# Kernel tuning notes

Hardware: AMD Instinct MI355X
Metric: run time of the kernel (lower is better)

Reference implementation:

```python
import jax, jax.numpy as jnp
import numpy as np

_EPS = 1e-5
_I48 = float(1.0 / np.sqrt(48.0))
_I16 = float(1.0 / np.sqrt(16.0))
# fully-connected TP paths (mul_in, mul_out) for hidden(48x0e+48x1o+16x1e) x sh(0e+1e+2e) -> hidden
_PATHS = [(48, 48), (48, 16), (48, 48), (48, 48), (48, 48), (16, 16), (16, 48), (16, 16), (16, 16)]
_NW = sum(i * o for i, o in _PATHS)  # 11520


def _ln(x, g, b):
    mu = x.mean(-1, keepdims=True)
    var = ((x - mu) ** 2).mean(-1, keepdims=True)
    return g * (x - mu) * jax.lax.rsqrt(var + _EPS) + b


def _split(W):
    out, off = [], 0
    for i, o in _PATHS:
        out.append(W[:, off:off + i * o].reshape(-1, i, o))
        off += i * o
    return out


def _forward(protein_coords, protein_features, ligand_coords, ligand_features, t,
             te_w1, te_b1, te_w2, te_b2, te_ln_g, te_ln_b,
             pe_w1, pe_b1, pe_ln_g, pe_ln_b, pe_w2, pe_b2,
             le_w1, le_b1, le_ln_g, le_ln_b, le_w2, le_b2,
             sp_w, sp_b, emb_w, ee_w1, ee_b1, ee_w2, ee_b2,
             conv_w1, conv_b1, conv_w2, conv_b2, conv_w3, conv_b3,
             bn_gs, bn_bs, bn_gv, bn_gw, si_ws, si_wv, si_ww,
             out_ws, out_wv, edge_src, edge_dst):
    Nl = ligand_coords.shape[0]
    Np = protein_coords.shape[0]
    N = Nl + Np
    E = edge_src.shape[0]
    silu = jax.nn.silu

    # sinusoidal time embedding -> Linear/SiLU/Linear/LayerNorm
    half = 32
    freq = jnp.exp(jnp.arange(half, dtype=jnp.float32) * (-np.log(10000.0) / (half - 1)))
    emb = t[:, None] * freq[None, :]
    emb = jnp.concatenate([jnp.sin(emb), jnp.cos(emb)], -1)  # (1, 64)
    temb = _ln(silu(emb @ te_w1 + te_b1) @ te_w2 + te_b2, te_ln_g, te_ln_b)

    # scalar node encoders (dropout = eval identity)
    protein_ca = protein_coords[:, 0, :]
    ph = silu(_ln(protein_features @ pe_w1 + pe_b1, pe_ln_g, pe_ln_b)) @ pe_w2 + pe_b2
    lh = silu(_ln(ligand_features @ le_w1 + le_b1, le_ln_g, le_ln_b)) @ le_w2 + le_b2

    # edge geometry (ligand -> protein) + spherical harmonics in Cartesian form
    vec = ligand_coords[edge_src] - protein_ca[edge_dst]  # (E, 3)
    dist = jnp.sqrt((vec ** 2).sum(-1) + 1e-12)
    n = vec / dist[:, None]  # unit vector = l=1 SH
    Q = n[:, :, None] * n[:, None, :] - jnp.eye(3, dtype=n.dtype) / 3.0  # l=2 SH (traceless sym)
    te_exp = jnp.broadcast_to(temb[0], (E, temb.shape[-1]))
    ef = silu(jnp.concatenate([dist[:, None], te_exp], -1) @ ee_w1 + ee_b1) @ ee_w2 + ee_b2  # (E, 32)

    # input embedding: scalars only feed 0e; 1o/1e channels start at zero
    comb = jnp.concatenate([lh, ph], 0) @ sp_w + sp_b  # (N, 48)
    s = (comb @ emb_w) * _I48
    v = jnp.zeros((N, 48, 3), s.dtype)
    w = jnp.zeros((N, 16, 3), s.dtype)

    dst_n = edge_dst + Nl
    deg = jax.ops.segment_sum(jnp.ones((E,), s.dtype), dst_n, N).clip(1.0)

    for i in range(conv_w1.shape[0]):
        # edge MLP -> per-edge fully-connected tensor-product weights
        m = silu(ef @ conv_w1[i] + conv_b1[i])
        m = silu(m @ conv_w2[i] + conv_b2[i])
        Wt = m @ conv_w3[i] + conv_b3[i]  # (E, 11520)
        Wss, Wsw, Wv0, Wv1, Wv2, Ww0, Wws, Ww1, Ww2 = _split(Wt)

        se, ve, we = s[edge_src], v[edge_src], w[edge_src]
        wn = jnp.einsum('eid,ed->ei', we, n)        # 1e x 1e -> 0e (dot)
        cv = jnp.cross(ve, n[:, None, :])           # 1o x 1e -> 1o (cross)
        cw = jnp.cross(we, n[:, None, :])           # 1e x 1e -> 1e (cross)
        qv = jnp.einsum('edc,eic->eid', Q, ve)      # 1o x 2e -> 1o
        qw = jnp.einsum('edc,eic->eid', Q, we)      # 1e x 2e -> 1e

        m_s = jnp.einsum('eio,ei->eo', Wss, se) * _I48 + jnp.einsum('eio,ei->eo', Wws, wn) * _I16
        m_v = (jnp.einsum('eio,eid->eod', Wv0, ve) + jnp.einsum('eio,eid->eod', Wv1, cv)
               + jnp.einsum('eio,eid->eod', Wv2, qv)) * _I48
        m_w = jnp.einsum('eio,ei,ed->eod', Wsw, se, n) * _I48 + (
            jnp.einsum('eio,eid->eod', Ww0, we) + jnp.einsum('eio,eid->eod', Ww1, cw)
            + jnp.einsum('eio,eid->eod', Ww2, qw)) * _I16

        # scatter-mean to destination nodes
        S = jax.ops.segment_sum(m_s, dst_n, N) / deg[:, None]
        V = jax.ops.segment_sum(m_v, dst_n, N) / deg[:, None, None]
        Wm = jax.ops.segment_sum(m_w, dst_n, N) / deg[:, None, None]

        # self interaction (per-irrep linear)
        a_s = S + (s @ si_ws[i]) * _I48
        a_v = V + jnp.einsum('io,nid->nod', si_wv[i], v) * _I48
        a_w = Wm + jnp.einsum('io,nid->nod', si_ww[i], w) * _I16

        # equivariant batch norm (batch statistics)
        mu = a_s.mean(0)
        var = ((a_s - mu) ** 2).mean(0)
        n_s = bn_gs[i] * (a_s - mu) * jax.lax.rsqrt(var + _EPS) + bn_bs[i]
        n_v = a_v * (bn_gv[i] * jax.lax.rsqrt((a_v ** 2).sum(-1).mean(0) + _EPS))[None, :, None]
        n_w = a_w * (bn_gw[i] * jax.lax.rsqrt((a_w ** 2).sum(-1).mean(0) + _EPS))[None, :, None]

        s, v, w = s + n_s, v + n_v, w + n_w

    feats = (s[:Nl] @ out_ws) * _I48                          # (Nl, 256)
    out_v = jnp.einsum('io,nid->nod', out_wv, v[:Nl]) * _I48  # (Nl, 3, 3)
    vf = out_v.mean(1)                                        # vector_field (Nl, 3)
    return jnp.concatenate([vf, feats], -1)                   # (Nl, 259)


def setup_inputs():
    key = jax.random.key(0)
    ks = iter(jax.random.split(key, 80))
    f32 = jnp.float32

    def nrm(shape, scale=1.0):
        return jax.random.normal(next(ks), shape, f32) * scale

    def lin(fi, fo, lead=()):
        return nrm(lead + (fi, fo), 1.0 / np.sqrt(fi)), jnp.zeros(lead + (fo,), f32)

    Nl, Np, E, L = 2048, 4096, 8192, 6
    inp = {}
    inp['protein_coords'] = nrm((Np, 2, 3), 5.0)
    inp['protein_features'] = nrm((Np, 96))
    inp['ligand_coords'] = nrm((Nl, 3), 5.0)
    inp['ligand_features'] = nrm((Nl, 52))
    inp['t'] = jax.random.uniform(next(ks), (1,), f32)
    inp['te_w1'], inp['te_b1'] = lin(64, 128)
    inp['te_w2'], inp['te_b2'] = lin(128, 64)
    inp['te_ln_g'], inp['te_ln_b'] = jnp.ones((64,), f32), jnp.zeros((64,), f32)
    inp['pe_w1'], inp['pe_b1'] = lin(96, 128)
    inp['pe_ln_g'], inp['pe_ln_b'] = jnp.ones((128,), f32), jnp.zeros((128,), f32)
    inp['pe_w2'], inp['pe_b2'] = lin(128, 48)
    inp['le_w1'], inp['le_b1'] = lin(52, 128)
    inp['le_ln_g'], inp['le_ln_b'] = jnp.ones((128,), f32), jnp.zeros((128,), f32)
    inp['le_w2'], inp['le_b2'] = lin(128, 48)
    inp['sp_w'], inp['sp_b'] = lin(48, 48)
    inp['emb_w'] = nrm((48, 48))
    inp['ee_w1'], inp['ee_b1'] = lin(65, 32)
    inp['ee_w2'], inp['ee_b2'] = lin(32, 32)
    inp['conv_w1'], inp['conv_b1'] = lin(32, 128, (L,))
    inp['conv_w2'], inp['conv_b2'] = lin(128, 128, (L,))
    inp['conv_w3'], inp['conv_b3'] = lin(128, _NW, (L,))
    inp['bn_gs'], inp['bn_bs'] = jnp.ones((L, 48), f32), jnp.zeros((L, 48), f32)
    inp['bn_gv'], inp['bn_gw'] = jnp.ones((L, 48), f32), jnp.ones((L, 16), f32)
    inp['si_ws'] = nrm((L, 48, 48))
    inp['si_wv'] = nrm((L, 48, 48))
    inp['si_ww'] = nrm((L, 16, 16))
    inp['out_ws'] = nrm((48, 256))
    inp['out_wv'] = nrm((48, 3))
    inp['edge_src'] = jax.random.randint(next(ks), (E,), 0, Nl)
    inp['edge_dst'] = jax.random.randint(next(ks), (E,), 0, Np)
    return inp


def reference(protein_coords, protein_features, ligand_coords, ligand_features, t,
              te_w1, te_b1, te_w2, te_b2, te_ln_g, te_ln_b,
              pe_w1, pe_b1, pe_ln_g, pe_ln_b, pe_w2, pe_b2,
              le_w1, le_b1, le_ln_g, le_ln_b, le_w2, le_b2,
              sp_w, sp_b, emb_w, ee_w1, ee_b1, ee_w2, ee_b2,
              conv_w1, conv_b1, conv_w2, conv_b2, conv_w3, conv_b3,
              bn_gs, bn_bs, bn_gv, bn_gw, si_ws, si_wv, si_ww,
              out_ws, out_wv, edge_src, edge_dst):
    return _forward(protein_coords, protein_features, ligand_coords, ligand_features, t,
                    te_w1, te_b1, te_w2, te_b2, te_ln_g, te_ln_b,
                    pe_w1, pe_b1, pe_ln_g, pe_ln_b, pe_w2, pe_b2,
                    le_w1, le_b1, le_ln_g, le_ln_b, le_w2, le_b2,
                    sp_w, sp_b, emb_w, ee_w1, ee_b1, ee_w2, ee_b2,
                    conv_w1, conv_b1, conv_w2, conv_b2, conv_w3, conv_b3,
                    bn_gs, bn_bs, bn_gv, bn_gw, si_ws, si_wv, si_ww,
                    out_ws, out_wv, edge_src, edge_dst)
```

## Files before the change

kernel.cpp:

```cpp
#include <hip/hip_runtime.h>
#include <hip/hip_bf16.h>
#include <math.h>

#define I48 0.14433756729740643f
#define NKB 194
#define KCH 4
#define KSPL 6

typedef __attribute__((ext_vector_type(8))) _Float16 half8;
typedef __attribute__((ext_vector_type(4))) float f32x4;

__device__ __forceinline__ float silu_f(float x){ return x / (1.f + __expf(-x)); }

__global__ void k_temb(const float* __restrict__ t_in,
                       const float* __restrict__ w1, const float* __restrict__ b1,
                       const float* __restrict__ w2, const float* __restrict__ b2,
                       const float* __restrict__ g,  const float* __restrict__ b,
                       float* __restrict__ temb){
  __shared__ float emb[64], h1[128], red[128];
  __shared__ float s_mu, s_rs;
  int t = threadIdx.x;
  float tv = t_in[0];
  if (t < 64){
    int i = t & 31;
    float fr = __expf((float)i * (-9.210340371976184f/31.f));
    float a = tv * fr;
    emb[t] = (t < 32) ? sinf(a) : cosf(a);
  }
  __syncthreads();
  {
    float z = b1[t];
    for (int i=0;i<64;i++) z += emb[i]*w1[i*128+t];
    h1[t] = silu_f(z);
  }
  __syncthreads();
  float tp = 0.f;
  if (t < 64){
    tp = b2[t];
    for (int j=0;j<128;j++) tp += h1[j]*w2[j*64+t];
  }
  red[t] = (t<64)? tp : 0.f;
  __syncthreads();
  for (int st=64;st;st>>=1){ if(t<st) red[t]+=red[t+st]; __syncthreads(); }
  if (t==0) s_mu = red[0]/64.f;
  __syncthreads();
  float d = tp - s_mu;
  red[t] = (t<64)? d*d : 0.f;
  __syncthreads();
  for (int st=64;st;st>>=1){ if(t<st) red[t]+=red[t+st]; __syncthreads(); }
  if (t==0) s_rs = rsqrtf(red[0]/64.f + 1e-5f);
  __syncthreads();
  if (t<64) temb[t] = g[t]*(d*s_rs) + b[t];
}

__global__ void k_encs0(const float* __restrict__ x, int in_dim,
                        const float* __restrict__ w1, const float* __restrict__ b1,
                        const float* __restrict__ g,  const float* __restrict__ bb,
                        const float* __restrict__ w2, const float* __restrict__ b2,
                        const float* __restrict__ spw, const float* __restrict__ spb,
                        const float* __restrict__ embw,
                        float* __restrict__ s, int row_off){
  __shared__ float sx[96], sh[128], red[128], vout[48], c48[48];
  __shared__ float s_mu, s_rs;
  int row = blockIdx.x, t = threadIdx.x;
  for (int i=t;i<in_dim;i+=128) sx[i] = x[(size_t)row*in_dim+i];
  __syncthreads();
  float z = b1[t];
  for (int i=0;i<in_dim;i++) z += sx[i]*w1[i*128+t];
  red[t]=z; __syncthreads();
  for (int st=64;st;st>>=1){ if(t<st) red[t]+=red[t+st]; __syncthreads(); }
  if(!t) s_mu = red[0]/128.f;
  __syncthreads();
  float d = z - s_mu;
  red[t]=d*d; __syncthreads();
  for (int st=64;st;st>>=1){ if(t<st) red[t]+=red[t+st]; __syncthreads(); }
  if(!t) s_rs = rsqrtf(red[0]/128.f+1e-5f);
  __syncthreads();
  float h = g[t]*(d*s_rs)+bb[t];
  sh[t] = silu_f(h);
  __syncthreads();
  if (t<48){
    float o = b2[t];
    for (int j=0;j<128;j++) o += sh[j]*w2[j*48+t];
    vout[t] = o;
  }
  __syncthreads();
  if (t<48){
    float c = spb[t];
    for (int i=0;i<48;i++) c += vout[i]*spw[i*48+t];
    c48[t] = c;
  }
  __syncthreads();
  if (t<48){
    float v = 0.f;
    for (int i=0;i<48;i++) v += c48[i]*embw[i*48+t];
    s[(size_t)(row_off+row)*48+t] = v*I48;
  }
}

__global__ void k_edge(const float* __restrict__ lc, const float* __restrict__ pc,
                       const int* __restrict__ src, const int* __restrict__ dst,
                       const float* __restrict__ temb,
                       const float* __restrict__ w1, const float* __restrict__ b1,
                       const float* __restrict__ w2, const float* __restrict__ b2,
                       float* __restrict__ ef, float* __restrict__ degf,
                       int E, int Nl){
  __shared__ float sh_h[2][32];
  int t = threadIdx.x, sub = t>>5, j = t&31;
  int e = blockIdx.x*2 + sub;
  if (e < E){
    int s_ = src[e], d_ = dst[e];
    float vx = lc[(size_t)s_*3+0]-pc[(size_t)d_*6+0];
    float vy = lc[(size_t)s_*3+1]-pc[(size_t)d_*6+1];
    float vz = lc[(size_t)s_*3+2]-pc[(size_t)d_*6+2];
    float dist = sqrtf(vx*vx+vy*vy+vz*vz+1e-12f);
    float h = b1[j] + dist*w1[j];
    for (int a=0;a<64;a++) h += temb[a]*w1[(a+1)*32+j];
    sh_h[sub][j] = silu_f(h);
  }
  __syncthreads();
  if (e < E){
    float o = b2[j];
    for (int a=0;a<32;a++) o += sh_h[sub][a]*w2[a*32+j];
    ef[(size_t)e*32+j] = o;
    if (j==0) atomicAdd(&degf[Nl + dst[e]], 1.f);
  }
}

__global__ void k_packMLP(const float* __restrict__ w1, const float* __restrict__ w2,
                          _Float16* __restrict__ w1p, _Float16* __restrict__ w2p, int L){
  int tot1 = L*8*512;
  int tot2 = L*32*512;
  int total = tot1 + tot2;
  for (int idx = blockIdx.x*blockDim.x+threadIdx.x; idx < total; idx += gridDim.x*blockDim.x){
    if (idx < tot1){
      int j = idx & 7, lane = (idx>>3)&63, rest = idx>>9;
      int nt = rest & 7, l = rest >> 3;
      int k = (lane>>4)*8 + j, o = nt*16 + (lane&15);
      w1p[idx] = (_Float16)w1[((size_t)l*32 + k)*128 + o];
    } else {
      int i2 = idx - tot1;
      int j = i2 & 7, lane = (i2>>3)&63, rest = i2>>9;
      int nt = rest & 7, kb = (rest>>3)&3, l = rest >> 5;
      int k = kb*32 + (lane>>4)*8 + j, o = nt*16 + (lane&15);
      w2p[i2] = (_Float16)w2[((size_t)l*128 + k)*128 + o];
    }
  }
}

__global__ __launch_bounds__(256) void k_mlp2(
    const float* __restrict__ ef,
    const _Float16* __restrict__ w1p, const float* __restrict__ b1a,
    const _Float16* __restrict__ w2p, const float* __restrict__ b2a,
    _Float16* __restrict__ m2h, int E){
  __shared__ __align__(16) _Float16 sef[64][40];
  __shared__ __align__(16) _Float16 shh[64][136];
  __shared__ float sb1[128], sb2[128];
  const int t = threadIdx.x, lane = t & 63, w = t >> 6;
  const int e0 = blockIdx.x * 64;
  const int l  = blockIdx.y;
  const _Float16* w1l = w1p + (size_t)l*4096;
  const _Float16* w2l = w2p + (size_t)l*16384;
  if (t < 128) sb1[t] = b1a[l*128 + t];
  else         sb2[t-128] = b2a[l*128 + (t-128)];
  {
    int row = t >> 2, g = t & 3;
    const float* p = ef + ((size_t)(e0+row))*32 + g*8;
    float4 p0 = *(const float4*)p, p1 = *(const float4*)(p+4);
    half8 hv;
    hv[0]=(_Float16)p0.x; hv[1]=(_Float16)p0.y; hv[2]=(_Float16)p0.z; hv[3]=(_Float16)p0.w;
    hv[4]=(_Float16)p1.x; hv[5]=(_Float16)p1.y; hv[6]=(_Float16)p1.z; hv[7]=(_Float16)p1.w;
    *(half8*)&sef[row][g*8] = hv;
  }
  __syncthreads();
  const int m = lane & 15, quad = lane >> 4;
  const int r = w*16 + m;
  half8 a1 = *(const half8*)&sef[r][quad*8];
  f32x4 acc1[8];
  #pragma unroll
  for (int nt=0; nt<8; nt++){
    half8 b = *(const half8*)(w1l + (nt*64 + lane)*8);
    f32x4 z = {0.f,0.f,0.f,0.f};
    acc1[nt] = __builtin_amdgcn_mfma_f32_16x16x32_f16(a1, b, z, 0,0,0);
  }
  #pragma unroll
  for (int nt=0; nt<8; nt++){
    float bv = sb1[nt*16 + m];
    #pragma unroll
    for (int rr=0; rr<4; rr++)
      shh[w*16 + quad*4 + rr][nt*16 + m] = (_Float16)silu_f(acc1[nt][rr] + bv);
  }
  __syncthreads();
  f32x4 acc2[8];
  #pragma unroll
  for (int nt=0;nt<8;nt++) acc2[nt] = (f32x4){0.f,0.f,0.f,0.f};
  #pragma unroll
  for (int kb=0; kb<4; kb++){
    half8 a2 = *(const half8*)&shh[r][kb*32 + quad*8];
    #pragma unroll
    for (int nt=0; nt<8; nt++){
      half8 b = *(const half8*)(w2l + ((size_t)(kb*8+nt)*64 + lane)*8);
      acc2[nt] = __builtin_amdgcn_mfma_f32_16x16x32_f16(a2, b, acc2[nt], 0,0,0);
    }
  }
  __syncthreads();
  #pragma unroll
  for (int nt=0; nt<8; nt++){
    float bv = sb2[nt*16 + m];
    #pragma unroll
    for (int rr=0; rr<4; rr++)
      shh[w*16 + quad*4 + rr][nt*16 + m] = (_Float16)silu_f(acc2[nt][rr] + bv);
  }
  __syncthreads();
  for (int q = t; q < 64*16; q += 256){
    int row = q >> 4, c = q & 15;
    half8 hv = *(const half8*)&shh[row][c*8];
    *(half8*)(m2h + ((size_t)l*E + e0 + row)*128 + c*8) = hv;
  }
}

__global__ void k_packB2(const float* __restrict__ w3, const float* __restrict__ b3,
                         _Float16* __restrict__ wbh, int L){
  int tot1 = L*128*2304;
  int tot2 = L*64*48;
  int total = tot1 + tot2;
  for (int idx = blockIdx.x*blockDim.x+threadIdx.x; idx < total; idx += gridDim.x*blockDim.x){
    if (idx < tot1){
      int r = idx % 2304; int q = idx / 2304;
      int kk = q & 127;   int l = q >> 7;
      float v = w3[(size_t)(l*128+kk)*11520 + r];
      int i = r / 48, o = r - i*48;
      int kp = i*128 + kk;
      int kblk = kp >> 5, p = kp & 31;
      int lane = ((p>>3)<<4) + (o & 15);
      int j = p & 7;
      int nt = o >> 4;
      wbh[((((size_t)l*NKB + kblk)*3 + nt)*64 + lane)*8 + j] = (_Float16)v;
    } else {
      int i2 = idx - tot1;
      int o = i2 % 48; int q = i2 / 48;
      int ii = q & 63; int l = q >> 6;
      float v = (ii < 48) ? b3[(size_t)l*11520 + ii*48 + o] : 0.f;
      int kp = 6144 + ii;
      int kblk = kp >> 5, p = kp & 31;
      int lane = ((p>>3)<<4) + (o & 15);
      int j = p & 7;
      int nt = o >> 4;
      wbh[((((size_t)l*NKB + kblk)*3 + nt)*64 + lane)*8 + j] = (_Float16)v;
    }
  }
}

__global__ __launch_bounds__(256) void k_msg6(
    const _Float16* __restrict__ m2h, const float* __restrict__ s,
    const float* __restrict__ a_s, const float* __restrict__ bnlp,
    const float* __restrict__ gp, const float* __restrict__ bp, int apply, int N,
    const _Float16* __restrict__ wbh,
    const int* __restrict__ src, const int* __restrict__ dst,
    float* __restrict__ Sacc, int Nl){
  __shared__ __align__(16) _Float16 sB[2][KCH*1536];
  __shared__ __align__(16) _Float16 sseq[128][72];
  __shared__ int sdst[128];
  __shared__ float ksc[48], kbs[48];
  const int t = threadIdx.x, lane = t & 63, w = t >> 6;
  const int e0 = blockIdx.x * 128;
  const int by = blockIdx.y;
  const int kb0 = by*32;
  const int kb1 = (by==KSPL-1) ? NKB : kb0+32;

  if (t < 48){
    if (apply){
      float su = bnlp[t], sq = bnlp[48+t];
      float mu  = su/(float)N;
      float var = sq/(float)N - mu*mu;
      float r = rsqrtf(var + 1e-5f);
      float sc = gp[t]*r;
      ksc[t] = sc; kbs[t] = bp[t] - mu*sc;
    } else { ksc[t]=0.f; kbs[t]=0.f; }
  }
  if (t < 128) sdst[t] = dst[e0+t];
  __syncthreads();

  for (int q = t; q < 128*9; q += 256){
    int e = q/9, g = q - e*9;
    half8 hv = {};
    if (g < 6){
      size_t base = (size_t)src[e0+e]*48 + g*8;
      const float* sp = s + base;
      if (apply){
        const float* ap = a_s + base;
        #pragma unroll
        for (int j=0;j<8;j++){
          int o = g*8+j;
          hv[j] = (_Float16)(sp[j] + ap[j]*ksc[o] + kbs[o]);
        }
      } else {
        #pragma unroll
        for (int j=0;j<8;j++) hv[j] = (_Float16)sp[j];
      }
    }
    *(half8*)&sseq[e][g*8] = hv;
  }

  const int m = lane & 15, quad = lane >> 4;
  const int r0 = w*32 + m, r1 = r0 + 16;

  half8 f0[4], f1[4];
  {
    const _Float16* base0 = m2h + (size_t)(e0+r0)*128 + quad*8;
    const _Float16* base1 = m2h + (size_t)(e0+r1)*128 + quad*8;
    #pragma unroll
    for (int sub=0; sub<4; sub++){
      f0[sub] = *(const half8*)(base0 + sub*32);
      f1[sub] = *(const half8*)(base1 + sub*32);
    }
  }

  auto stage = [&](int c){
    int kbase = kb0 + c*KCH;
    int nk = kb1 - kbase; if (nk > KCH) nk = KCH;
    int bytes = nk*3072;
    const char* g = (const char*)wbh + (size_t)kbase*3072;
    char* lb = (char*)sB[c&1];
    for (int off = w*1024; off < bytes; off += 4096){
      __builtin_amdgcn_global_load_lds(
        (const __attribute__((address_space(1))) void*)(g + off + (size_t)lane*16),
        (__attribute__((address_space(3))) void*)(lb + off), 16, 0, 0);
    }
  };
  stage(0);

  f32x4 acc00={0.f,0.f,0.f,0.f}, acc01={0.f,0.f,0.f,0.f}, acc02={0.f,0.f,0.f,0.f};
  f32x4 acc10={0.f,0.f,0.f,0.f}, acc11={0.f,0.f,0.f,0.f}, acc12={0.f,0.f,0.f,0.f};

  const int nch = (kb1-kb0+KCH-1)/KCH;
  for (int c = 0; c < nch; c++){
    __syncthreads();
    if (c+1 < nch) stage(c+1);
    int kbase = kb0 + c*KCH;
    int kbn = kb1 - kbase; if (kbn > KCH) kbn = KCH;
    const _Float16* bb = sB[c&1];
    if (kbn == KCH && kbase < 192){
      int i = kbase >> 2;
      _Float16 sv0 = sseq[r0][i], sv1 = sseq[r1][i];
      half8 s0v = {sv0,sv0,sv0,sv0,sv0,sv0,sv0,sv0};
      half8 s1v = {sv1,sv1,sv1,sv1,sv1,sv1,sv1,sv1};
      #pragma unroll
      for (int kk = 0; kk < KCH; kk++){
        half8 a0 = f0[kk] * s0v;
        half8 a1 = f1[kk] * s1v;
        const _Float16* bk = bb + kk*1536 + lane*8;
        half8 b0 = *(const half8*)(bk);
        half8 b1 = *(const half8*)(bk + 512);
        half8 b2 = *(const half8*)(bk + 1024);
        acc00 = __builtin_amdgcn_mfma_f32_16x16x32_f16(a0, b0, acc00, 0, 0, 0);
        acc01 = __builtin_amdgcn_mfma_f32_16x16x32_f16(a0, b1, acc01, 0, 0, 0);
        acc02 = __builtin_amdgcn_mfma_f32_16x16x32_f16(a0, b2, acc02, 0, 0, 0);
        acc10 = __builtin_amdgcn_mfma_f32_16x16x32_f16(a1, b0, acc10, 0, 0, 0);
        acc11 = __builtin_amdgcn_mfma_f32_16x16x32_f16(a1, b1, acc11, 0, 0, 0);
        acc12 = __builtin_amdgcn_mfma_f32_16x16x32_f16(a1, b2, acc12, 0, 0, 0);
      }
    } else {
      for (int kk = 0; kk < kbn; kk++){
        int kblk = kbase + kk;
        int ib = ((kblk-192) << 5) + quad*8;
        half8 a0 = *(const half8*)&sseq[r0][ib];
        half8 a1 = *(const half8*)&sseq[r1][ib];
        const _Float16* bk = bb + kk*1536 + lane*8;
        half8 b0 = *(const half8*)(bk);
        half8 b1 = *(const half8*)(bk + 512);
        half8 b2 = *(const half8*)(bk + 1024);
        acc00 = __builtin_amdgcn_mfma_f32_16x16x32_f16(a0, b0, acc00, 0, 0, 0);
        acc01 = __builtin_amdgcn_mfma_f32_16x16x32_f16(a0, b1, acc01, 0, 0, 0);
        acc02 = __builtin_amdgcn_mfma_f32_16x16x32_f16(a0, b2, acc02, 0, 0, 0);
        acc10 = __builtin_amdgcn_mfma_f32_16x16x32_f16(a1, b0, acc10, 0, 0, 0);
        acc11 = __builtin_amdgcn_mfma_f32_16x16x32_f16(a1, b1, acc11, 0, 0, 0);
        acc12 = __builtin_amdgcn_mfma_f32_16x16x32_f16(a1, b2, acc12, 0, 0, 0);
      }
    }
  }
  #pragma unroll
  for (int r = 0; r < 4; r++){
    int el0 = w*32 + quad*4 + r;
    int el1 = el0 + 16;
    float* p0 = Sacc + (size_t)(Nl + sdst[el0])*48 + m;
    float* p1 = Sacc + (size_t)(Nl + sdst[el1])*48 + m;
    atomicAdd(p0 +  0, acc00[r]*I48);
    atomicAdd(p0 + 16, acc01[r]*I48);
    atomicAdd(p0 + 32, acc02[r]*I48);
    atomicAdd(p1 +  0, acc10[r]*I48);
    atomicAdd(p1 + 16, acc11[r]*I48);
    atomicAdd(p1 + 32, acc12[r]*I48);
  }
}

__global__ __launch_bounds__(256) void k_node3(float* __restrict__ Sacc,
                       const float* __restrict__ degf,
                       float* __restrict__ s, const float* __restrict__ siw,
                       float* __restrict__ a_s,
                       const float* __restrict__ bnlp, const float* __restrict__ gp,
                       const float* __restrict__ bp, int apply,
                       float* __restrict__ bnl, int N){
  __shared__ float sh_s[16][48];
  __shared__ float sw[2304];
  __shared__ float csum[48], csq[48];
  __shared__ float ksc[48], kbs[48];
  int t = threadIdx.x;
  int n0 = blockIdx.x*16;
  if (t < 48){
    if (apply){
      float su = bnlp[t], sq = bnlp[48+t];
      float mu  = su/(float)N;
      float var = sq/(float)N - mu*mu;
      float r = rsqrtf(var + 1e-5f);
      float sc = gp[t]*r;
      ksc[t] = sc; kbs[t] = bp[t] - mu*sc;
    } else { ksc[t]=0.f; kbs[t]=0.f; }
    csum[t]=0.f; csq[t]=0.f;
  }
  for (int q=t;q<2304;q+=256) sw[q] = siw[q];
  __syncthreads();
  for (int q=t;q<768;q+=256){
    int nl=q/48, o=q-nl*48;
    size_t idx = (size_t)(n0+nl)*48+o;
    float v = s[idx];
    if (apply){
      v += a_s[idx]*ksc[o] + kbs[o];
      s[idx] = v;
    }
    sh_s[nl][o] = v;
  }
  __syncthreads();
  int nl = t>>4;
  int ob = (t&15)*3;
  int n = n0+nl;
  float dg = degf[n]; if (dg < 1.f) dg = 1.f;
  float inv = 1.f/dg;
  #pragma unroll
  for (int j=0;j<3;j++){
    int o = ob+j;
    size_t idx = (size_t)n*48+o;
    float acc = 0.f;
    for (int i=0;i<48;i++) acc += sh_s[nl][i]*sw[i*48+o];
    float a = Sacc[idx]*inv + acc*I48;
    Sacc[idx] = 0.f;
    a_s[idx] = a;
    atomicAdd(&csum[o], a);
    atomicAdd(&csq[o], a*a);
  }
  __syncthreads();
  if (t<96) atomicAdd(&bnl[t], (t<48) ? csum[t] : csq[t-48]);
}

__global__ void k_out2(const float* __restrict__ s, const float* __restrict__ a_s,
                       const float* __restrict__ bnlp, const float* __restrict__ gp,
                       const float* __restrict__ bp, int N,
                       const float* __restrict__ ows, float* __restrict__ out){
  __shared__ float sh_s[48];
  __shared__ float ksc[48], kbs[48];
  int n = blockIdx.x, t = threadIdx.x;
  if (t < 48){
    float su = bnlp[t], sq = bnlp[48+t];
    float mu  = su/(float)N;
    float var = sq/(float)N - mu*mu;
    float r = rsqrtf(var + 1e-5f);
    float sc = gp[t]*r;
    ksc[t] = sc; kbs[t] = bp[t] - mu*sc;
  }
  __syncthreads();
  if (t<48){
    size_t idx = (size_t)n*48+t;
    sh_s[t] = s[idx] + a_s[idx]*ksc[t] + kbs[t];
  }
  __syncthreads();
  float acc = 0.f;
  for (int i=0;i<48;i++) acc += sh_s[i]*ows[i*256+t];
  out[(size_t)n*259 + 3 + t] = acc*I48;
  if (t<3) out[(size_t)n*259 + t] = 0.f;
}

extern "C" void kernel_launch(void* const* d_in, const int* in_sizes, int n_in,
                              void* d_out, int out_size, void* d_ws, size_t ws_size,
                              hipStream_t stream){
  const float* protein_coords   = (const float*)d_in[0];
  const float* protein_features = (const float*)d_in[1];
  const float* ligand_coords    = (const float*)d_in[2];
  const float* ligand_features  = (const float*)d_in[3];
  const float* t_in    = (const float*)d_in[4];
  const float* te_w1   = (const float*)d_in[5];
  const float* te_b1   = (const float*)d_in[6];
  const float* te_w2   = (const float*)d_in[7];
  const float* te_b2   = (const float*)d_in[8];
  const float* te_ln_g = (const float*)d_in[9];
  const float* te_ln_b = (const float*)d_in[10];
  const float* pe_w1   = (const float*)d_in[11];
  const float* pe_b1   = (const float*)d_in[12];
  const float* pe_ln_g = (const float*)d_in[13];
  const float* pe_ln_b = (const float*)d_in[14];
  const float* pe_w2   = (const float*)d_in[15];
  const float* pe_b2   = (const float*)d_in[16];
  const float* le_w1   = (const float*)d_in[17];
  const float* le_b1   = (const float*)d_in[18];
  const float* le_ln_g = (const float*)d_in[19];
  const float* le_ln_b = (const float*)d_in[20];
  const float* le_w2   = (const float*)d_in[21];
  const float* le_b2   = (const float*)d_in[22];
  const float* sp_w    = (const float*)d_in[23];
  const float* sp_b    = (const float*)d_in[24];
  const float* emb_w   = (const float*)d_in[25];
  const float* ee_w1   = (const float*)d_in[26];
  const float* ee_b1   = (const float*)d_in[27];
  const float* ee_w2   = (const float*)d_in[28];
  const float* ee_b2   = (const float*)d_in[29];
  const float* conv_w1 = (const float*)d_in[30];
  const float* conv_b1 = (const float*)d_in[31];
  const float* conv_w2 = (const float*)d_in[32];
  const float* conv_b2 = (const float*)d_in[33];
  const float* conv_w3 = (const float*)d_in[34];
  const float* conv_b3 = (const float*)d_in[35];
  const float* bn_gs   = (const float*)d_in[36];
  const float* bn_bs   = (const float*)d_in[37];
  const float* si_ws   = (const float*)d_in[40];
  const float* out_ws  = (const float*)d_in[43];
  const int* edge_src  = (const int*)d_in[45];
  const int* edge_dst  = (const int*)d_in[46];

  int Np = in_sizes[0]/6;
  int Nl = in_sizes[2]/3;
  int E  = in_sizes[45];
  int N  = Nl+Np;
  int L  = in_sizes[36]/48;

  float* W = (float*)d_ws;
  size_t off = 0;
  auto alloc = [&](size_t n)->float*{ float* p = W+off; off += (n+63)&~(size_t)63; return p; };
  float* degf  = alloc(N);
  float* Sacc  = alloc((size_t)N*48);
  float* bnb   = alloc((size_t)L*96);
  float* temb  = alloc(64);
  float* sbuf  = alloc((size_t)N*48);
  float* ef    = alloc((size_t)E*32);
  float* a_s   = alloc((size_t)N*48);
  _Float16* m2h = (_Float16*)alloc((size_t)L*E*128/2 + 64);
  _Float16* wbh = (_Float16*)alloc((size_t)L*NKB*1536/2 + 64);
  _Float16* w1p = (_Float16*)alloc((size_t)L*4096/2 + 64);
  _Float16* w2p = (_Float16*)alloc((size_t)L*16384/2 + 64);

  hipMemsetAsync(degf, 0, ((size_t)N + (size_t)N*48 + (size_t)L*96 + 192)*sizeof(float), stream);
  k_packB2<<<2048,256,0,stream>>>(conv_w3, conv_b3, wbh, L);
  k_packMLP<<<480,256,0,stream>>>(conv_w1, conv_w2, w1p, w2p, L);
  k_temb<<<1,128,0,stream>>>(t_in, te_w1, te_b1, te_w2, te_b2, te_ln_g, te_ln_b, temb);
  k_encs0<<<Np,128,0,stream>>>(protein_features, 96, pe_w1, pe_b1, pe_ln_g, pe_ln_b,
                               pe_w2, pe_b2, sp_w, sp_b, emb_w, sbuf, Nl);
  k_encs0<<<Nl,128,0,stream>>>(ligand_features, 52, le_w1, le_b1, le_ln_g, le_ln_b,
                               le_w2, le_b2, sp_w, sp_b, emb_w, sbuf, 0);
  k_edge<<<(E+1)/2,64,0,stream>>>(ligand_coords, protein_coords, edge_src, edge_dst, temb,
                                  ee_w1, ee_b1, ee_w2, ee_b2, ef, degf, E, Nl);
  dim3 mlpg(E/64, L);
  k_mlp2<<<mlpg,256,0,stream>>>(ef, w1p, conv_b1, w2p, conv_b2, m2h, E);

  dim3 mgrid(E/128, KSPL);
  for (int l=0;l<L;l++){
    const float* bnlp = (l>0) ? (bnb + (l-1)*96) : bnb;
    const float* gp   = (l>0) ? (bn_gs + (l-1)*48) : bn_gs;
    const float* bp   = (l>0) ? (bn_bs + (l-1)*48) : bn_bs;
    int apply = (l>0) ? 1 : 0;
    k_msg6<<<mgrid,256,0,stream>>>(m2h + (size_t)l*E*128, sbuf, a_s, bnlp, gp, bp, apply, N,
                                   wbh + (size_t)l*NKB*1536, edge_src, edge_dst, Sacc, Nl);
    k_node3<<<N/16,256,0,stream>>>(Sacc, degf, sbuf, si_ws + (size_t)l*2304, a_s,
                                   bnlp, gp, bp, apply, bnb + l*96, N);
  }
  k_out2<<<Nl,256,0,stream>>>(sbuf, a_s, bnb + (L-1)*96, bn_gs + (L-1)*48, bn_bs + (L-1)*48,
                              N, out_ws, (float*)d_out);
}
```

Before: 463.1 us.

## Halve message-kernel edge tile and merge pack and encoder launches

The message kernel now processes 64 edges per block instead of 128, with one 16-row MFMA tile per wave, which doubles the grid and lowers register and LDS use per block. Two weight-packing kernels are merged into one launch, and the protein and ligand encoders become a single launch that selects weights per row. This trades more parallel blocks and fewer launches for twice the staging of the B weights per edge, since each weight chunk is now reused across fewer edges.

```diff
diff --git a/kernel.cpp b/kernel.cpp
--- a/kernel.cpp
+++ b/kernel.cpp
@@ -53,17 +53,28 @@
   if (t<64) temb[t] = g[t]*(d*s_rs) + b[t];
 }
 
-__global__ void k_encs0(const float* __restrict__ x, int in_dim,
-                        const float* __restrict__ w1, const float* __restrict__ b1,
-                        const float* __restrict__ g,  const float* __restrict__ bb,
-                        const float* __restrict__ w2, const float* __restrict__ b2,
-                        const float* __restrict__ spw, const float* __restrict__ spb,
-                        const float* __restrict__ embw,
-                        float* __restrict__ s, int row_off){
+__global__ void k_encall(const float* __restrict__ pf, const float* __restrict__ lf, int Nl,
+    const float* __restrict__ pw1, const float* __restrict__ pb1,
+    const float* __restrict__ pg,  const float* __restrict__ pbb,
+    const float* __restrict__ pw2, const float* __restrict__ pb2,
+    const float* __restrict__ lw1, const float* __restrict__ lb1,
+    const float* __restrict__ lg,  const float* __restrict__ lbb,
+    const float* __restrict__ lw2, const float* __restrict__ lb2,
+    const float* __restrict__ spw, const float* __restrict__ spb,
+    const float* __restrict__ embw, float* __restrict__ s){
   __shared__ float sx[96], sh[128], red[128], vout[48], c48[48];
   __shared__ float s_mu, s_rs;
   int row = blockIdx.x, t = threadIdx.x;
-  for (int i=t;i<in_dim;i+=128) sx[i] = x[(size_t)row*in_dim+i];
+  bool lig = row < Nl;
+  int in_dim = lig ? 52 : 96;
+  const float* x  = lig ? (lf + (size_t)row*52) : (pf + (size_t)(row-Nl)*96);
+  const float* w1 = lig ? lw1 : pw1;
+  const float* b1 = lig ? lb1 : pb1;
+  const float* g  = lig ? lg  : pg;
+  const float* bb = lig ? lbb : pbb;
+  const float* w2 = lig ? lw2 : pw2;
+  const float* b2 = lig ? lb2 : pb2;
+  for (int i=t;i<in_dim;i+=128) sx[i] = x[i];
   __syncthreads();
   float z = b1[t];
   for (int i=0;i<in_dim;i++) z += sx[i]*w1[i*128+t];
@@ -94,7 +105,7 @@
   if (t<48){
     float v = 0.f;
     for (int i=0;i<48;i++) v += c48[i]*embw[i*48+t];
-    s[(size_t)(row_off+row)*48+t] = v*I48;
+    s[(size_t)row*48+t] = v*I48;
   }
 }
 
@@ -127,23 +138,50 @@
   }
 }
 
-__global__ void k_packMLP(const float* __restrict__ w1, const float* __restrict__ w2,
+__global__ void k_packAll(const float* __restrict__ w3, const float* __restrict__ b3,
+                          const float* __restrict__ w1, const float* __restrict__ w2,
+                          _Float16* __restrict__ wbh,
                           _Float16* __restrict__ w1p, _Float16* __restrict__ w2p, int L){
-  int tot1 = L*8*512;
-  int tot2 = L*32*512;
-  int total = tot1 + tot2;
+  int tot1 = L*128*2304;
+  int tot2 = L*64*48;
+  int tot3 = L*8*512;
+  int tot4 = L*32*512;
+  int total = tot1 + tot2 + tot3 + tot4;
   for (int idx = blockIdx.x*blockDim.x+threadIdx.x; idx < total; idx += gridDim.x*blockDim.x){
     if (idx < tot1){
-      int j = idx & 7, lane = (idx>>3)&63, rest = idx>>9;
+      int r = idx % 2304; int q = idx / 2304;
+      int kk = q & 127;   int l = q >> 7;
+      float v = w3[(size_t)(l*128+kk)*11520 + r];
+      int i = r / 48, o = r - i*48;
+      int kp = i*128 + kk;
+      int kblk = kp >> 5, p = kp & 31;
+      int lane = ((p>>3)<<4) + (o & 15);
+      int j = p & 7;
+      int nt = o >> 4;
+      wbh[((((size_t)l*NKB + kblk)*3 + nt)*64 + lane)*8 + j] = (_Float16)v;
+    } else if (idx < tot1 + tot2){
+      int i2 = idx - tot1;
+      int o = i2 % 48; int q = i2 / 48;
+      int ii = q & 63; int l = q >> 6;
+      float v = (ii < 48) ? b3[(size_t)l*11520 + ii*48 + o] : 0.f;
+      int kp = 6144 + ii;
+      int kblk = kp >> 5, p = kp & 31;
+      int lane = ((p>>3)<<4) + (o & 15);
+      int j = p & 7;
+      int nt = o >> 4;
+      wbh[((((size_t)l*NKB + kblk)*3 + nt)*64 + lane)*8 + j] = (_Float16)v;
+    } else if (idx < tot1 + tot2 + tot3){
+      int i3 = idx - tot1 - tot2;
+      int j = i3 & 7, lane = (i3>>3)&63, rest = i3>>9;
       int nt = rest & 7, l = rest >> 3;
       int k = (lane>>4)*8 + j, o = nt*16 + (lane&15);
-      w1p[idx] = (_Float16)w1[((size_t)l*32 + k)*128 + o];
+      w1p[i3] = (_Float16)w1[((size_t)l*32 + k)*128 + o];
     } else {
-      int i2 = idx - tot1;
-      int j = i2 & 7, lane = (i2>>3)&63, rest = i2>>9;
+      int i4 = idx - tot1 - tot2 - tot3;
+      int j = i4 & 7, lane = (i4>>3)&63, rest = i4>>9;
       int nt = rest & 7, kb = (rest>>3)&3, l = rest >> 5;
       int k = kb*32 + (lane>>4)*8 + j, o = nt*16 + (lane&15);
-      w2p[i2] = (_Float16)w2[((size_t)l*128 + k)*128 + o];
+      w2p[i4] = (_Float16)w2[((size_t)l*128 + k)*128 + o];
     }
   }
 }
@@ -219,39 +257,7 @@
   }
 }
 
-__global__ void k_packB2(const float* __restrict__ w3, const float* __restrict__ b3,
-                         _Float16* __restrict__ wbh, int L){
-  int tot1 = L*128*2304;
-  int tot2 = L*64*48;
-  int total = tot1 + tot2;
-  for (int idx = blockIdx.x*blockDim.x+threadIdx.x; idx < total; idx += gridDim.x*blockDim.x){
-    if (idx < tot1){
-      int r = idx % 2304; int q = idx / 2304;
-      int kk = q & 127;   int l = q >> 7;
-      float v = w3[(size_t)(l*128+kk)*11520 + r];
-      int i = r / 48, o = r - i*48;
-      int kp = i*128 + kk;
-      int kblk = kp >> 5, p = kp & 31;
-      int lane = ((p>>3)<<4) + (o & 15);
-      int j = p & 7;
-      int nt = o >> 4;
-      wbh[((((size_t)l*NKB + kblk)*3 + nt)*64 + lane)*8 + j] = (_Float16)v;
-    } else {
-      int i2 = idx - tot1;
-      int o = i2 % 48; int q = i2 / 48;
-      int ii = q & 63; int l = q >> 6;
-      float v = (ii < 48) ? b3[(size_t)l*11520 + ii*48 + o] : 0.f;
-      int kp = 6144 + ii;
-      int kblk = kp >> 5, p = kp & 31;
-      int lane = ((p>>3)<<4) + (o & 15);
-      int j = p & 7;
-      int nt = o >> 4;
-      wbh[((((size_t)l*NKB + kblk)*3 + nt)*64 + lane)*8 + j] = (_Float16)v;
-    }
-  }
-}
-
-__global__ __launch_bounds__(256) void k_msg6(
+__global__ __launch_bounds__(256) void k_msg7(
     const _Float16* __restrict__ m2h, const float* __restrict__ s,
     const float* __restrict__ a_s, const float* __restrict__ bnlp,
     const float* __restrict__ gp, const float* __restrict__ bp, int apply, int N,
@@ -259,11 +265,11 @@
     const int* __restrict__ src, const int* __restrict__ dst,
     float* __restrict__ Sacc, int Nl){
   __shared__ __align__(16) _Float16 sB[2][KCH*1536];
-  __shared__ __align__(16) _Float16 sseq[128][72];
-  __shared__ int sdst[128];
+  __shared__ __align__(16) _Float16 sseq[64][72];
+  __shared__ int sdst[64];
   __shared__ float ksc[48], kbs[48];
   const int t = threadIdx.x, lane = t & 63, w = t >> 6;
-  const int e0 = blockIdx.x * 128;
+  const int e0 = blockIdx.x * 64;
   const int by = blockIdx.y;
   const int kb0 = by*32;
   const int kb1 = (by==KSPL-1) ? NKB : kb0+32;
@@ -278,10 +284,10 @@
       ksc[t] = sc; kbs[t] = bp[t] - mu*sc;
     } else { ksc[t]=0.f; kbs[t]=0.f; }
   }
-  if (t < 128) sdst[t] = dst[e0+t];
-  __syncthreads();
-
-  for (int q = t; q < 128*9; q += 256){
+  if (t < 64) sdst[t] = dst[e0+t];
+  __syncthreads();
+
+  for (int q = t; q < 64*9; q += 256){
     int e = q/9, g = q - e*9;
     half8 hv = {};
     if (g < 6){
@@ -303,17 +309,13 @@
   }
 
   const int m = lane & 15, quad = lane >> 4;
-  const int r0 = w*32 + m, r1 = r0 + 16;
-
-  half8 f0[4], f1[4];
+  const int r0 = w*16 + m;
+
+  half8 f0[4];
   {
     const _Float16* base0 = m2h + (size_t)(e0+r0)*128 + quad*8;
-    const _Float16* base1 = m2h + (size_t)(e0+r1)*128 + quad*8;
     #pragma unroll
-    for (int sub=0; sub<4; sub++){
-      f0[sub] = *(const half8*)(base0 + sub*32);
-      f1[sub] = *(const half8*)(base1 + sub*32);
-    }
+    for (int sub=0; sub<4; sub++) f0[sub] = *(const half8*)(base0 + sub*32);
   }
 
   auto stage = [&](int c){
@@ -330,8 +332,7 @@
   };
   stage(0);
 
-  f32x4 acc00={0.f,0.f,0.f,0.f}, acc01={0.f,0.f,0.f,0.f}, acc02={0.f,0.f,0.f,0.f};
-  f32x4 acc10={0.f,0.f,0.f,0.f}, acc11={0.f,0.f,0.f,0.f}, acc12={0.f,0.f,0.f,0.f};
+  f32x4 acc0={0.f,0.f,0.f,0.f}, acc1={0.f,0.f,0.f,0.f}, acc2={0.f,0.f,0.f,0.f};
 
   const int nch = (kb1-kb0+KCH-1)/KCH;
   for (int c = 0; c < nch; c++){
@@ -342,55 +343,41 @@
     const _Float16* bb = sB[c&1];
     if (kbn == KCH && kbase < 192){
       int i = kbase >> 2;
-      _Float16 sv0 = sseq[r0][i], sv1 = sseq[r1][i];
+      _Float16 sv0 = sseq[r0][i];
       half8 s0v = {sv0,sv0,sv0,sv0,sv0,sv0,sv0,sv0};
-      half8 s1v = {sv1,sv1,sv1,sv1,sv1,sv1,sv1,sv1};
       #pragma unroll
       for (int kk = 0; kk < KCH; kk++){
         half8 a0 = f0[kk] * s0v;
-        half8 a1 = f1[kk] * s1v;
         const _Float16* bk = bb + kk*1536 + lane*8;
         half8 b0 = *(const half8*)(bk);
         half8 b1 = *(const half8*)(bk + 512);
         half8 b2 = *(const half8*)(bk + 1024);
-        acc00 = __builtin_amdgcn_mfma_f32_16x16x32_f16(a0, b0, acc00, 0, 0, 0);
-        acc01 = __builtin_amdgcn_mfma_f32_16x16x32_f16(a0, b1, acc01, 0, 0, 0);
-        acc02 = __builtin_amdgcn_mfma_f32_16x16x32_f16(a0, b2, acc02, 0, 0, 0);
-        acc10 = __builtin_amdgcn_mfma_f32_16x16x32_f16(a1, b0, acc10, 0, 0, 0);
-        acc11 = __builtin_amdgcn_mfma_f32_16x16x32_f16(a1, b1, acc11, 0, 0, 0);
-        acc12 = __builtin_amdgcn_mfma_f32_16x16x32_f16(a1, b2, acc12, 0, 0, 0);
+        acc0 = __builtin_amdgcn_mfma_f32_16x16x32_f16(a0, b0, acc0, 0, 0, 0);
+        acc1 = __builtin_amdgcn_mfma_f32_16x16x32_f16(a0, b1, acc1, 0, 0, 0);
+        acc2 = __builtin_amdgcn_mfma_f32_16x16x32_f16(a0, b2, acc2, 0, 0, 0);
       }
     } else {
       for (int kk = 0; kk < kbn; kk++){
         int kblk = kbase + kk;
         int ib = ((kblk-192) << 5) + quad*8;
         half8 a0 = *(const half8*)&sseq[r0][ib];
-        half8 a1 = *(const half8*)&sseq[r1][ib];
         const _Float16* bk = bb + kk*1536 + lane*8;
         half8 b0 = *(const half8*)(bk);
         half8 b1 = *(const half8*)(bk + 512);
         half8 b2 = *(const half8*)(bk + 1024);
-        acc00 = __builtin_amdgcn_mfma_f32_16x16x32_f16(a0, b0, acc00, 0, 0, 0);
-        acc01 = __builtin_amdgcn_mfma_f32_16x16x32_f16(a0, b1, acc01, 0, 0, 0);
-        acc02 = __builtin_amdgcn_mfma_f32_16x16x32_f16(a0, b2, acc02, 0, 0, 0);
-        acc10 = __builtin_amdgcn_mfma_f32_16x16x32_f16(a1, b0, acc10, 0, 0, 0);
-        acc11 = __builtin_amdgcn_mfma_f32_16x16x32_f16(a1, b1, acc11, 0, 0, 0);
-        acc12 = __builtin_amdgcn_mfma_f32_16x16x32_f16(a1, b2, acc12, 0, 0, 0);
+        acc0 = __builtin_amdgcn_mfma_f32_16x16x32_f16(a0, b0, acc0, 0, 0, 0);
+        acc1 = __builtin_amdgcn_mfma_f32_16x16x32_f16(a0, b1, acc1, 0, 0, 0);
+        acc2 = __builtin_amdgcn_mfma_f32_16x16x32_f16(a0, b2, acc2, 0, 0, 0);
       }
     }
   }
   #pragma unroll
   for (int r = 0; r < 4; r++){
-    int el0 = w*32 + quad*4 + r;
-    int el1 = el0 + 16;
+    int el0 = w*16 + quad*4 + r;
     float* p0 = Sacc + (size_t)(Nl + sdst[el0])*48 + m;
-    float* p1 = Sacc + (size_t)(Nl + sdst[el1])*48 + m;
-    atomicAdd(p0 +  0, acc00[r]*I48);
-    atomicAdd(p0 + 16, acc01[r]*I48);
-    atomicAdd(p0 + 32, acc02[r]*I48);
-    atomicAdd(p1 +  0, acc10[r]*I48);
-    atomicAdd(p1 + 16, acc11[r]*I48);
-    atomicAdd(p1 + 32, acc12[r]*I48);
+    atomicAdd(p0 +  0, acc0[r]*I48);
+    atomicAdd(p0 + 16, acc1[r]*I48);
+    atomicAdd(p0 + 32, acc2[r]*I48);
   }
 }
 
@@ -547,25 +534,24 @@
   _Float16* w2p = (_Float16*)alloc((size_t)L*16384/2 + 64);
 
   hipMemsetAsync(degf, 0, ((size_t)N + (size_t)N*48 + (size_t)L*96 + 192)*sizeof(float), stream);
-  k_packB2<<<2048,256,0,stream>>>(conv_w3, conv_b3, wbh, L);
-  k_packMLP<<<480,256,0,stream>>>(conv_w1, conv_w2, w1p, w2p, L);
+  k_packAll<<<2048,256,0,stream>>>(conv_w3, conv_b3, conv_w1, conv_w2, wbh, w1p, w2p, L);
   k_temb<<<1,128,0,stream>>>(t_in, te_w1, te_b1, te_w2, te_b2, te_ln_g, te_ln_b, temb);
-  k_encs0<<<Np,128,0,stream>>>(protein_features, 96, pe_w1, pe_b1, pe_ln_g, pe_ln_b,
-                               pe_w2, pe_b2, sp_w, sp_b, emb_w, sbuf, Nl);
-  k_encs0<<<Nl,128,0,stream>>>(ligand_features, 52, le_w1, le_b1, le_ln_g, le_ln_b,
-                               le_w2, le_b2, sp_w, sp_b, emb_w, sbuf, 0);
+  k_encall<<<N,128,0,stream>>>(protein_features, ligand_features, Nl,
+                               pe_w1, pe_b1, pe_ln_g, pe_ln_b, pe_w2, pe_b2,
+                               le_w1, le_b1, le_ln_g, le_ln_b, le_w2, le_b2,
+                               sp_w, sp_b, emb_w, sbuf);
   k_edge<<<(E+1)/2,64,0,stream>>>(ligand_coords, protein_coords, edge_src, edge_dst, temb,
                                   ee_w1, ee_b1, ee_w2, ee_b2, ef, degf, E, Nl);
   dim3 mlpg(E/64, L);
   k_mlp2<<<mlpg,256,0,stream>>>(ef, w1p, conv_b1, w2p, conv_b2, m2h, E);
 
-  dim3 mgrid(E/128, KSPL);
+  dim3 mgrid(E/64, KSPL);
   for (int l=0;l<L;l++){
     const float* bnlp = (l>0) ? (bnb + (l-1)*96) : bnb;
     const float* gp   = (l>0) ? (bn_gs + (l-1)*48) : bn_gs;
     const float* bp   = (l>0) ? (bn_bs + (l-1)*48) : bn_bs;
     int apply = (l>0) ? 1 : 0;
-    k_msg6<<<mgrid,256,0,stream>>>(m2h + (size_t)l*E*128, sbuf, a_s, bnlp, gp, bp, apply, N,
+    k_msg7<<<mgrid,256,0,stream>>>(m2h + (size_t)l*E*128, sbuf, a_s, bnlp, gp, bp, apply, N,
                                    wbh + (size_t)l*NKB*1536, edge_src, edge_dst, Sacc, Nl);
     k_node3<<<N/16,256,0,stream>>>(Sacc, degf, sbuf, si_ws + (size_t)l*2304, a_s,
                                    bnlp, gp, bp, apply, bnb + l*96, N);
```

Result: faster. 449.1 us (-3.0%).
